# Kernel optimization log

Measured on AMD Instinct MI355X. Metric: run time of the kernel, lower is better.

Reference implementation:

```python
import jax, jax.numpy as jnp
import numpy as np

RELU_NEG_SLOPE = 0.2

def _gat_layer(x, W, a, src, dst, num_nodes, concat):
    # x: [N, Din]; W: [H, Din, F]; a: [H, 2F]; src/dst: [E]
    H, _, F = W.shape
    proj = jnp.einsum('nd,hdf->nhf', x, W)              # [N, H, F]
    a_self, a_nb = a[:, :F], a[:, F:]                   # [H, F] each
    alpha_self = jnp.einsum('nhf,hf->nh', proj, a_self) # [N, H]
    alpha_nb = jnp.einsum('nhf,hf->nh', proj, a_nb)     # [N, H]
    # edge score: a . [proj_dst || proj_src], dst = center node i, src = neighbor j
    e = jax.nn.leaky_relu(alpha_self[dst] + alpha_nb[src], RELU_NEG_SLOPE)  # [E, H]
    e_max = jax.ops.segment_max(e, dst, num_segments=num_nodes)
    e_exp = jnp.exp(e - e_max[dst])
    denom = jax.ops.segment_sum(e_exp, dst, num_segments=num_nodes)
    w = e_exp / denom[dst]                              # [E, H] softmax per dst node
    msg = proj[src] * w[:, :, None]                     # [E, H, F]
    out = jax.ops.segment_sum(msg, dst, num_segments=num_nodes)  # [N, H, F]
    if concat:
        return out.reshape(num_nodes, H * F)
    return out.mean(axis=1)


def setup_inputs() -> dict:
    key = jax.random.key(0)
    k1, k2, k3, k4, k5, k6 = jax.random.split(key, 6)
    N, Din, F1, H1 = 10000, 128, 64, 8
    Dmid = H1 * F1  # 512
    F2, H2 = 64, 1
    x = jax.random.normal(k1, (N, Din), dtype=jnp.float32)
    edges = jax.random.randint(k2, (2, 80000), 0, N, dtype=jnp.int64)
    W1 = jax.random.normal(k3, (H1, Din, F1), dtype=jnp.float32) / np.sqrt(Din)
    a1 = jax.random.normal(k4, (H1, 2 * F1), dtype=jnp.float32) / np.sqrt(2 * F1)
    W2 = jax.random.normal(k5, (H2, Dmid, F2), dtype=jnp.float32) / np.sqrt(Dmid)
    a2 = jax.random.normal(k6, (H2, 2 * F2), dtype=jnp.float32) / np.sqrt(2 * F2)
    return {"x": x, "edges": edges, "W1": W1, "a1": a1, "W2": W2, "a2": a2}


def reference(x, edges, W1, a1, W2, a2):
    N = x.shape[0]
    loops = jnp.arange(N, dtype=edges.dtype)
    # undirected graph + self loops (Graph.neighborhood adds both directions and self)
    src = jnp.concatenate([edges[0], edges[1], loops])
    dst = jnp.concatenate([edges[1], edges[0], loops])
    h = _gat_layer(x, W1, a1, src, dst, N, concat=True)   # [N, 512]
    h = jax.nn.elu(h)
    out = _gat_layer(h, W2, a2, src, dst, N, concat=False)  # [N, 64]
    return out
```

## Files before the change

kernel.cpp:

```cpp
#include <hip/hip_runtime.h>
#include <hip/hip_fp16.h>

#define RELU_NEG_SLOPE 0.2f

typedef _Float16 half8 __attribute__((ext_vector_type(8)));
typedef float f32x4 __attribute__((ext_vector_type(4)));

__device__ __forceinline__ float leaky(float e) {
    return (e > 0.f) ? e : RELU_NEG_SLOPE * e;
}

__device__ __forceinline__ float elu1(float x) {
    return (x > 0.f) ? x : (__expf(x) - 1.f);
}

#define MAXN 16384
#define MAXPAD 16384

__device__ __align__(256) int            g_cnt[MAXN];
__device__ __align__(256) unsigned short g_ell[MAXN * 64];
__device__ __align__(256) __half         g_proj1p[(size_t)4 * MAXPAD * 128];
__device__ __align__(256) __half         g_W2t[64 * 512];
__device__ __align__(256) __half         g_proj2h[MAXN * 64];
__device__ __align__(256) float          g_as1[MAXN * 8];
__device__ __align__(256) float          g_an1[MAXN * 8];
__device__ __align__(256) float          g_as2[MAXN];
__device__ __align__(256) float          g_an2[MAXN];

__global__ __launch_bounds__(256) void k1_scatter_gemm1(
    const int* __restrict__ edges, int E0,
    const float* __restrict__ W2, int t2, int nscat,
    const float4* __restrict__ x4, const float* __restrict__ W1,
    const float* __restrict__ a1, int N, int slabN) {
    __shared__ __half Bs[64 * 132];
    if (blockIdx.x < nscat) {
        int i = blockIdx.x * 256 + threadIdx.x;
        if (i < 2 * E0) {
            int s = edges[i];
            int d = (i < E0) ? edges[E0 + i] : edges[i - E0];
            int pos = atomicAdd(&g_cnt[d], 1);
            g_ell[(d << 6) + pos] = (unsigned short)s;
        } else if (i < 2 * E0 + t2) {
            int j = i - 2 * E0;
            int f = j & 63;
            int d = j >> 6;
            g_W2t[f * 512 + d] = __float2half(W2[j]);
        }
        return;
    }
    int bid2 = blockIdx.x - nscat;
    const int h = bid2 & 7;
    const int by = bid2 >> 3;

    {
        const float4* W1h = (const float4*)W1 + h * 2048;
        int t = threadIdx.x;
#pragma unroll
        for (int r = 0; r < 8; r++) {
            int j4 = t + r * 256;
            float4 w = W1h[j4];
            int f = (j4 << 2) & 63;
            int d = j4 >> 4;
            Bs[(f + 0) * 132 + d] = __float2half(w.x);
            Bs[(f + 1) * 132 + d] = __float2half(w.y);
            Bs[(f + 2) * 132 + d] = __float2half(w.z);
            Bs[(f + 3) * 132 + d] = __float2half(w.w);
        }
    }
    __syncthreads();

    const int lane = threadIdx.x & 63;
    const int wave = threadIdx.x >> 6;
    const int q = lane >> 4;
    const int l15 = lane & 15;
    const int mrow = by * 64 + wave * 16;

    int arow = mrow + l15;
    if (arow >= N) arow = N - 1;
    const float4* Ar = x4 + (size_t)arow * 32;

    f32x4 acc[4] = {{0.f, 0.f, 0.f, 0.f}, {0.f, 0.f, 0.f, 0.f},
                    {0.f, 0.f, 0.f, 0.f}, {0.f, 0.f, 0.f, 0.f}};
#pragma unroll
    for (int ks = 0; ks < 4; ks++) {
        float4 a0 = Ar[ks * 8 + q * 2];
        float4 a1v = Ar[ks * 8 + q * 2 + 1];
        half8 av;
        av[0] = (_Float16)a0.x; av[1] = (_Float16)a0.y;
        av[2] = (_Float16)a0.z; av[3] = (_Float16)a0.w;
        av[4] = (_Float16)a1v.x; av[5] = (_Float16)a1v.y;
        av[6] = (_Float16)a1v.z; av[7] = (_Float16)a1v.w;
#pragma unroll
        for (int t = 0; t < 4; t++) {
            half8 bv = *(const half8*)(Bs + (t * 16 + l15) * 132 + q * 8 + ks * 32);
            acc[t] = __builtin_amdgcn_mfma_f32_16x16x32_f16(av, bv, acc[t], 0, 0, 0);
        }
    }

    __half* Cs = g_proj1p + (size_t)(h >> 1) * slabN + (h & 1) * 64;
    float asc[4], anc[4];
#pragma unroll
    for (int t = 0; t < 4; t++) {
        asc[t] = a1[h * 128 + t * 16 + l15];
        anc[t] = a1[h * 128 + 64 + t * 16 + l15];
    }
#pragma unroll
    for (int r = 0; r < 4; r++) {
        int mg = mrow + q * 4 + r;
        float ps = 0.f, pn = 0.f;
#pragma unroll
        for (int t = 0; t < 4; t++) {
            float v = acc[t][r];
            ps += v * asc[t];
            pn += v * anc[t];
            if (mg < N)
                Cs[(size_t)mg * 128 + t * 16 + l15] = __float2half(v);
        }
#pragma unroll
        for (int m = 8; m >= 1; m >>= 1) {
            ps += __shfl_xor(ps, m, 64);
            pn += __shfl_xor(pn, m, 64);
        }
        if (l15 == 0 && mg < N) {
            g_as1[mg * 8 + h] = ps;
            g_an1[mg * 8 + h] = pn;
        }
    }
}

__global__ __launch_bounds__(256) void k23_agg1_gemm2(
    const float* __restrict__ a2, int N, int slabN) {
    __shared__ __half hb[16][520];
    __shared__ float red[4][16][2];
    const int node0 = blockIdx.x * 16;
    const int wave = threadIdx.x >> 6;
    const int lane = threadIdx.x & 63;

    const int hp = wave;
    const int sub = lane >> 3;
    const int inner = lane & 7;
    const int hh = inner >> 2;
    const int h = hp * 2 + hh;
    const int c16 = (inner & 3) * 16;
    const __half* slab = g_proj1p + (size_t)hp * slabN;

    for (int nl = 0; nl < 16; nl++) {
        int d = node0 + nl;
        if (d >= N) break;
        int deg = g_cnt[d];
        const unsigned short* row = g_ell + (d << 6);
        float asd = g_as1[d * 8 + h];

        float acc[16];
#pragma unroll
        for (int i = 0; i < 16; i++) acc[i] = 0.f;
        float den = 0.f;
        if (sub == 0) {
            float e = __expf(leaky(asd + g_an1[d * 8 + h]));
            const __half* p = slab + (size_t)d * 128 + hh * 64 + c16;
            half8 v0 = *(const half8*)p;
            half8 v1 = *(const half8*)(p + 8);
            den = e;
#pragma unroll
            for (int i = 0; i < 8; i++) {
                acc[i] = e * (float)v0[i];
                acc[8 + i] = e * (float)v1[i];
            }
        }
        for (int j0 = 0; j0 < deg; j0 += 8) {
            int j = j0 + sub;
            int jc = (j < deg) ? j : (deg - 1);
            int s = row[jc];
            float e = __expf(leaky(asd + g_an1[s * 8 + h]));
            if (j >= deg) e = 0.f;
            const __half* p = slab + (size_t)s * 128 + hh * 64 + c16;
            half8 v0 = *(const half8*)p;
            half8 v1 = *(const half8*)(p + 8);
            den += e;
#pragma unroll
            for (int i = 0; i < 8; i++) {
                acc[i] += e * (float)v0[i];
                acc[8 + i] += e * (float)v1[i];
            }
        }
#pragma unroll
        for (int off = 32; off >= 8; off >>= 1) {
#pragma unroll
            for (int i = 0; i < 16; i++) acc[i] += __shfl_down(acc[i], off, 64);
            den += __shfl_down(den, off, 64);
        }
        if (sub == 0) {
            float r = 1.f / den;
            half8 o0, o1;
#pragma unroll
            for (int i = 0; i < 8; i++) {
                o0[i] = (_Float16)elu1(acc[i] * r);
                o1[i] = (_Float16)elu1(acc[8 + i] * r);
            }
            __half* op = &hb[nl][h * 64 + c16];
            *(half8*)op = o0;
            *(half8*)(op + 8) = o1;
        }
    }
    __syncthreads();

    const int q = lane >> 4;
    const int l15 = lane & 15;
    f32x4 acc2 = {0.f, 0.f, 0.f, 0.f};
    const __half* Bp = g_W2t + (size_t)(wave * 16 + l15) * 512 + q * 8;
#pragma unroll
    for (int ks = 0; ks < 16; ks++) {
        half8 av = *(const half8*)&hb[l15][ks * 32 + q * 8];
        half8 bv = *(const half8*)(Bp + ks * 32);
        acc2 = __builtin_amdgcn_mfma_f32_16x16x32_f16(av, bv, acc2, 0, 0, 0);
    }
    float asc = a2[wave * 16 + l15];
    float anc = a2[64 + wave * 16 + l15];
#pragma unroll
    for (int r = 0; r < 4; r++) {
        int mg = node0 + q * 4 + r;
        float v = acc2[r];
        float ps = v * asc, pn = v * anc;
#pragma unroll
        for (int m = 8; m >= 1; m >>= 1) {
            ps += __shfl_xor(ps, m, 64);
            pn += __shfl_xor(pn, m, 64);
        }
        if (mg < N)
            g_proj2h[(size_t)mg * 64 + wave * 16 + l15] = __float2half(v);
        if (l15 == 0) {
            red[wave][q * 4 + r][0] = ps;
            red[wave][q * 4 + r][1] = pn;
        }
    }
    __syncthreads();
    if (threadIdx.x < 16) {
        int mg = node0 + threadIdx.x;
        if (mg < N) {
            int i = threadIdx.x;
            g_as2[mg] = red[0][i][0] + red[1][i][0] + red[2][i][0] + red[3][i][0];
            g_an2[mg] = red[0][i][1] + red[1][i][1] + red[2][i][1] + red[3][i][1];
        }
    }
}

__global__ __launch_bounds__(256) void agg_node_h1(float* __restrict__ out,
                                                   int N) {
    int d = blockIdx.x * 4 + (threadIdx.x >> 6);
    int lane = threadIdx.x & 63;
    if (d >= N) return;
    int sub = lane >> 3;
    int inner = lane & 7;
    int deg = g_cnt[d];
    if (lane == 0) g_cnt[d] = 0;
    const unsigned short* row = g_ell + (d << 6);
    float asd = g_as2[d];

    float acc[8];
#pragma unroll
    for (int i = 0; i < 8; i++) acc[i] = 0.f;
    float den = 0.f;
    for (int j0 = 0; j0 < deg; j0 += 8) {
        int j = j0 + sub;
        int jc = (j < deg) ? j : (deg - 1);
        int s = row[jc];
        float e = __expf(leaky(asd + g_an2[s]));
        if (j >= deg) e = 0.f;
        half8 v = *(const half8*)(g_proj2h + (size_t)s * 64 + inner * 8);
        den += e;
#pragma unroll
        for (int i = 0; i < 8; i++) acc[i] += e * (float)v[i];
    }

#pragma unroll
    for (int off = 32; off >= 8; off >>= 1) {
#pragma unroll
        for (int i = 0; i < 8; i++) acc[i] += __shfl_down(acc[i], off, 64);
        den += __shfl_down(den, off, 64);
    }

    if (sub == 0) {
        float e = __expf(leaky(asd + g_an2[d]));
        half8 v = *(const half8*)(g_proj2h + (size_t)d * 64 + inner * 8);
        den += e;
#pragma unroll
        for (int i = 0; i < 8; i++) acc[i] += e * (float)v[i];
        float rden = 1.f / den;
        float4 r0, r1;
        r0.x = acc[0] * rden; r0.y = acc[1] * rden;
        r0.z = acc[2] * rden; r0.w = acc[3] * rden;
        r1.x = acc[4] * rden; r1.y = acc[5] * rden;
        r1.z = acc[6] * rden; r1.w = acc[7] * rden;
        float* op = out + (size_t)d * 64 + inner * 8;
        *(float4*)op = r0;
        *(float4*)(op + 4) = r1;
    }
}

extern "C" void kernel_launch(void* const* d_in, const int* in_sizes, int n_in,
                              void* d_out, int out_size, void* d_ws, size_t ws_size,
                              hipStream_t stream) {
    const float* x  = (const float*)d_in[0];
    const int* edges = (const int*)d_in[1];
    const float* W1 = (const float*)d_in[2];
    const float* a1 = (const float*)d_in[3];
    const float* W2 = (const float*)d_in[4];
    const float* a2 = (const float*)d_in[5];

    const int Din = 128, H1 = 8, F = 64, Dmid = 512;
    const int N = in_sizes[0] / Din;
    const int E0 = in_sizes[1] / 2;
    const int Mpad = (N + 63) & ~63;
    const int slabN = Mpad * 128;
    (void)Dmid; (void)d_ws; (void)ws_size;

    int t2 = Dmid * F;
    int nscat = (2 * E0 + t2 + 255) / 256;
    int ngemm = H1 * (Mpad / 64);
    k1_scatter_gemm1<<<nscat + ngemm, 256, 0, stream>>>(
        edges, E0, W2, t2, nscat, (const float4*)x, W1, a1, N, slabN);

    k23_agg1_gemm2<<<(N + 15) / 16, 256, 0, stream>>>(a2, N, slabN);

    agg_node_h1<<<(N + 3) / 4, 256, 0, stream>>>((float*)d_out, N);
}
```

Measured before the change: 154.1 us.

## Split layer-1 aggregation and GEMM2 into separate kernels with wider edge batching

The fused aggregate-then-GEMM2 kernel, which walked 16 nodes serially per block, is split into a per-(node, head-pair) aggregation kernel that writes the ELU'd hidden state to a global fp16 buffer, plus a separate single-wave MFMA GEMM2 kernel. The split is meant to expose far more parallelism and shorten the serial per-block dependency chain. The gather loops in both aggregation kernels also now issue two to four neighbor loads before using them, to give more memory-level parallelism. In exchange there is an extra kernel launch and a round trip of the 512-wide hidden state through global memory.

Result: faster. 131.5 us (-14.6%).

```diff
diff --git a/kernel.cpp b/kernel.cpp
--- a/kernel.cpp
+++ b/kernel.cpp
@@ -20,6 +20,7 @@
 __device__ __align__(256) int            g_cnt[MAXN];
 __device__ __align__(256) unsigned short g_ell[MAXN * 64];
 __device__ __align__(256) __half         g_proj1p[(size_t)4 * MAXPAD * 128];
+__device__ __align__(256) __half         g_hbufh[(size_t)MAXPAD * 512];
 __device__ __align__(256) __half         g_W2t[64 * 512];
 __device__ __align__(256) __half         g_proj2h[MAXN * 64];
 __device__ __align__(256) float          g_as1[MAXN * 8];
@@ -128,118 +129,135 @@
     }
 }
 
-__global__ __launch_bounds__(256) void k23_agg1_gemm2(
-    const float* __restrict__ a2, int N, int slabN) {
-    __shared__ __half hb[16][520];
-    __shared__ float red[4][16][2];
-    const int node0 = blockIdx.x * 16;
-    const int wave = threadIdx.x >> 6;
-    const int lane = threadIdx.x & 63;
-
-    const int hp = wave;
+__global__ __launch_bounds__(256) void agg_h8_sliced(int N, int slabN) {
+    int bid = blockIdx.x;
+    int hp = bid & 3;
+    int rem = bid >> 2;
+    int d = rem * 4 + (threadIdx.x >> 6);
+    int lane = threadIdx.x & 63;
+    if (d >= N) return;
     const int sub = lane >> 3;
     const int inner = lane & 7;
     const int hh = inner >> 2;
     const int h = hp * 2 + hh;
     const int c16 = (inner & 3) * 16;
+
+    int deg = g_cnt[d];
+    const unsigned short* row = g_ell + (d << 6);
+    float asd = g_as1[d * 8 + h];
     const __half* slab = g_proj1p + (size_t)hp * slabN;
 
-    for (int nl = 0; nl < 16; nl++) {
-        int d = node0 + nl;
-        if (d >= N) break;
-        int deg = g_cnt[d];
-        const unsigned short* row = g_ell + (d << 6);
-        float asd = g_as1[d * 8 + h];
-
-        float acc[16];
-#pragma unroll
-        for (int i = 0; i < 16; i++) acc[i] = 0.f;
-        float den = 0.f;
-        if (sub == 0) {
-            float e = __expf(leaky(asd + g_an1[d * 8 + h]));
-            const __half* p = slab + (size_t)d * 128 + hh * 64 + c16;
-            half8 v0 = *(const half8*)p;
-            half8 v1 = *(const half8*)(p + 8);
-            den = e;
-#pragma unroll
-            for (int i = 0; i < 8; i++) {
-                acc[i] = e * (float)v0[i];
-                acc[8 + i] = e * (float)v1[i];
-            }
-        }
-        for (int j0 = 0; j0 < deg; j0 += 8) {
-            int j = j0 + sub;
-            int jc = (j < deg) ? j : (deg - 1);
-            int s = row[jc];
-            float e = __expf(leaky(asd + g_an1[s * 8 + h]));
-            if (j >= deg) e = 0.f;
-            const __half* p = slab + (size_t)s * 128 + hh * 64 + c16;
-            half8 v0 = *(const half8*)p;
-            half8 v1 = *(const half8*)(p + 8);
-            den += e;
-#pragma unroll
-            for (int i = 0; i < 8; i++) {
-                acc[i] += e * (float)v0[i];
-                acc[8 + i] += e * (float)v1[i];
-            }
-        }
-#pragma unroll
-        for (int off = 32; off >= 8; off >>= 1) {
-#pragma unroll
-            for (int i = 0; i < 16; i++) acc[i] += __shfl_down(acc[i], off, 64);
-            den += __shfl_down(den, off, 64);
-        }
-        if (sub == 0) {
-            float r = 1.f / den;
-            half8 o0, o1;
-#pragma unroll
-            for (int i = 0; i < 8; i++) {
-                o0[i] = (_Float16)elu1(acc[i] * r);
-                o1[i] = (_Float16)elu1(acc[8 + i] * r);
-            }
-            __half* op = &hb[nl][h * 64 + c16];
-            *(half8*)op = o0;
-            *(half8*)(op + 8) = o1;
-        }
-    }
-    __syncthreads();
-
+    float acc[16];
+#pragma unroll
+    for (int i = 0; i < 16; i++) acc[i] = 0.f;
+    float den = 0.f;
+    if (sub == 0) {
+        float e = __expf(leaky(asd + g_an1[d * 8 + h]));
+        const __half* p = slab + (size_t)d * 128 + hh * 64 + c16;
+        half8 v0 = *(const half8*)p;
+        half8 v1 = *(const half8*)(p + 8);
+        den = e;
+#pragma unroll
+        for (int i = 0; i < 8; i++) {
+            acc[i] = e * (float)v0[i];
+            acc[8 + i] = e * (float)v1[i];
+        }
+    }
+    for (int j0 = 0; j0 < deg; j0 += 16) {
+        int ja = j0 + sub;
+        int jb = ja + 8;
+        int jca = (ja < deg) ? ja : (deg - 1);
+        int jcb = (jb < deg) ? jb : (deg - 1);
+        int sa = row[jca];
+        int sb = row[jcb];
+        float na = g_an1[sa * 8 + h];
+        float nb = g_an1[sb * 8 + h];
+        const __half* pa = slab + (size_t)sa * 128 + hh * 64 + c16;
+        const __half* pb = slab + (size_t)sb * 128 + hh * 64 + c16;
+        half8 va0 = *(const half8*)pa;
+        half8 va1 = *(const half8*)(pa + 8);
+        half8 vb0 = *(const half8*)pb;
+        half8 vb1 = *(const half8*)(pb + 8);
+        float ea = __expf(leaky(asd + na));
+        float eb = __expf(leaky(asd + nb));
+        if (ja >= deg) ea = 0.f;
+        if (jb >= deg) eb = 0.f;
+        den += ea + eb;
+#pragma unroll
+        for (int i = 0; i < 8; i++) {
+            acc[i]     += ea * (float)va0[i] + eb * (float)vb0[i];
+            acc[8 + i] += ea * (float)va1[i] + eb * (float)vb1[i];
+        }
+    }
+
+#pragma unroll
+    for (int off = 32; off >= 8; off >>= 1) {
+#pragma unroll
+        for (int i = 0; i < 16; i++) acc[i] += __shfl_down(acc[i], off, 64);
+        den += __shfl_down(den, off, 64);
+    }
+
+    if (sub == 0) {
+        float r = 1.f / den;
+        half8 o0, o1;
+#pragma unroll
+        for (int i = 0; i < 8; i++) {
+            o0[i] = (_Float16)elu1(acc[i] * r);
+            o1[i] = (_Float16)elu1(acc[8 + i] * r);
+        }
+        __half* op = g_hbufh + (size_t)d * 512 + h * 64 + c16;
+        *(half8*)op = o0;
+        *(half8*)(op + 8) = o1;
+    }
+}
+
+__global__ __launch_bounds__(64) void mfma_gemm2(
+    const float* __restrict__ a2, int M) {
+    const int lane = threadIdx.x & 63;
     const int q = lane >> 4;
     const int l15 = lane & 15;
-    f32x4 acc2 = {0.f, 0.f, 0.f, 0.f};
-    const __half* Bp = g_W2t + (size_t)(wave * 16 + l15) * 512 + q * 8;
+    const int mrow = blockIdx.x * 16;
+
+    f32x4 acc[4] = {{0.f, 0.f, 0.f, 0.f}, {0.f, 0.f, 0.f, 0.f},
+                    {0.f, 0.f, 0.f, 0.f}, {0.f, 0.f, 0.f, 0.f}};
+    const __half* Ap = g_hbufh + (size_t)(mrow + l15) * 512 + q * 8;
+    const __half* Bp = g_W2t + (size_t)l15 * 512 + q * 8;
 #pragma unroll
     for (int ks = 0; ks < 16; ks++) {
-        half8 av = *(const half8*)&hb[l15][ks * 32 + q * 8];
-        half8 bv = *(const half8*)(Bp + ks * 32);
-        acc2 = __builtin_amdgcn_mfma_f32_16x16x32_f16(av, bv, acc2, 0, 0, 0);
-    }
-    float asc = a2[wave * 16 + l15];
-    float anc = a2[64 + wave * 16 + l15];
+        half8 av = *(const half8*)(Ap + ks * 32);
+#pragma unroll
+        for (int t = 0; t < 4; t++) {
+            half8 bv = *(const half8*)(Bp + (size_t)t * 16 * 512 + ks * 32);
+            acc[t] = __builtin_amdgcn_mfma_f32_16x16x32_f16(av, bv, acc[t], 0, 0, 0);
+        }
+    }
+
+    float asc[4], anc[4];
+#pragma unroll
+    for (int t = 0; t < 4; t++) {
+        asc[t] = a2[t * 16 + l15];
+        anc[t] = a2[64 + t * 16 + l15];
+    }
 #pragma unroll
     for (int r = 0; r < 4; r++) {
-        int mg = node0 + q * 4 + r;
-        float v = acc2[r];
-        float ps = v * asc, pn = v * anc;
+        int mg = mrow + q * 4 + r;
+        float ps = 0.f, pn = 0.f;
+#pragma unroll
+        for (int t = 0; t < 4; t++) {
+            float v = acc[t][r];
+            ps += v * asc[t];
+            pn += v * anc[t];
+            if (mg < M)
+                g_proj2h[(size_t)mg * 64 + t * 16 + l15] = __float2half(v);
+        }
 #pragma unroll
         for (int m = 8; m >= 1; m >>= 1) {
             ps += __shfl_xor(ps, m, 64);
             pn += __shfl_xor(pn, m, 64);
         }
-        if (mg < N)
-            g_proj2h[(size_t)mg * 64 + wave * 16 + l15] = __float2half(v);
-        if (l15 == 0) {
-            red[wave][q * 4 + r][0] = ps;
-            red[wave][q * 4 + r][1] = pn;
-        }
-    }
-    __syncthreads();
-    if (threadIdx.x < 16) {
-        int mg = node0 + threadIdx.x;
-        if (mg < N) {
-            int i = threadIdx.x;
-            g_as2[mg] = red[0][i][0] + red[1][i][0] + red[2][i][0] + red[3][i][0];
-            g_an2[mg] = red[0][i][1] + red[1][i][1] + red[2][i][1] + red[3][i][1];
+        if (l15 == 0 && mg < M) {
+            g_as2[mg] = ps;
+            g_an2[mg] = pn;
         }
     }
 }
@@ -260,16 +278,29 @@
 #pragma unroll
     for (int i = 0; i < 8; i++) acc[i] = 0.f;
     float den = 0.f;
-    for (int j0 = 0; j0 < deg; j0 += 8) {
-        int j = j0 + sub;
-        int jc = (j < deg) ? j : (deg - 1);
-        int s = row[jc];
-        float e = __expf(leaky(asd + g_an2[s]));
-        if (j >= deg) e = 0.f;
-        half8 v = *(const half8*)(g_proj2h + (size_t)s * 64 + inner * 8);
-        den += e;
-#pragma unroll
-        for (int i = 0; i < 8; i++) acc[i] += e * (float)v[i];
+    for (int j0 = 0; j0 < deg; j0 += 32) {
+        int jj[4], s[4];
+        float en[4];
+        half8 v[4];
+#pragma unroll
+        for (int g = 0; g < 4; g++) {
+            jj[g] = j0 + g * 8 + sub;
+            int jc = (jj[g] < deg) ? jj[g] : (deg - 1);
+            s[g] = row[jc];
+        }
+#pragma unroll
+        for (int g = 0; g < 4; g++) en[g] = g_an2[s[g]];
+#pragma unroll
+        for (int g = 0; g < 4; g++)
+            v[g] = *(const half8*)(g_proj2h + (size_t)s[g] * 64 + inner * 8);
+#pragma unroll
+        for (int g = 0; g < 4; g++) {
+            float e = __expf(leaky(asd + en[g]));
+            if (jj[g] >= deg) e = 0.f;
+            den += e;
+#pragma unroll
+            for (int i = 0; i < 8; i++) acc[i] += e * (float)v[g][i];
+        }
     }
 
 #pragma unroll
@@ -307,20 +338,23 @@
     const float* W2 = (const float*)d_in[4];
     const float* a2 = (const float*)d_in[5];
 
-    const int Din = 128, H1 = 8, F = 64, Dmid = 512;
+    const int Din = 128, H1 = 8, Dmid = 512;
     const int N = in_sizes[0] / Din;
     const int E0 = in_sizes[1] / 2;
     const int Mpad = (N + 63) & ~63;
     const int slabN = Mpad * 128;
-    (void)Dmid; (void)d_ws; (void)ws_size;
-
-    int t2 = Dmid * F;
+    (void)d_ws; (void)ws_size;
+
+    int t2 = Dmid * 64;
     int nscat = (2 * E0 + t2 + 255) / 256;
     int ngemm = H1 * (Mpad / 64);
     k1_scatter_gemm1<<<nscat + ngemm, 256, 0, stream>>>(
         edges, E0, W2, t2, nscat, (const float4*)x, W1, a1, N, slabN);
 
-    k23_agg1_gemm2<<<(N + 15) / 16, 256, 0, stream>>>(a2, N, slabN);
+    int nbp = (N + 3) / 4;
+    agg_h8_sliced<<<4 * nbp, 256, 0, stream>>>(N, slabN);
+
+    mfma_gemm2<<<(N + 15) / 16, 64, 0, stream>>>(a2, N);
 
     agg_node_h1<<<(N + 3) / 4, 256, 0, stream>>>((float*)d_out, N);
 }
```
